# Kernel tuning notes

Hardware: AMD Instinct MI355X
Metric: run time of the kernel (lower is better)

## Reference

```python
import jax, jax.numpy as jnp
import numpy as np

SPAN = 20
REPEAT = 90


def setup_inputs() -> dict:
    key = jax.random.key(0)
    k1, k2 = jax.random.split(key)
    B, C, H, W = 4, 1, 512, 512
    pred = jax.random.normal(k1, (B, C, H, W), dtype=jnp.float32)
    gt = jax.random.normal(k2, (B, C, H, W), dtype=jnp.float32)
    # random offsets: magnitude in [1, span], random sign (matches np.random logic in torch module)
    rng = np.random.default_rng(0)
    mag_h = rng.integers(1, SPAN + 1, size=REPEAT)
    mag_w = rng.integers(1, SPAN + 1, size=REPEAT)
    sign_h = np.where(rng.uniform(size=REPEAT) > 0.5, -1, 1)
    sign_w = np.where(rng.uniform(size=REPEAT) > 0.5, -1, 1)
    h_offsets = jnp.asarray(mag_h * sign_h, dtype=jnp.int32)
    w_offsets = jnp.asarray(mag_w * sign_w, dtype=jnp.int32)
    return {"pred": pred, "gt": gt, "h_offsets": h_offsets, "w_offsets": w_offsets}


def _relative_depth(x, h_offsets, w_offsets):
    """x: [B,C,H,W] -> [B,Hb,Wb,R*C] stack of base-block minus shifted-block diffs."""
    B, C, H, W = x.shape
    Hb, Wb = H - 2 * SPAN, W - 2 * SPAN
    base = jax.lax.dynamic_slice(x, (0, 0, SPAN, SPAN), (B, C, Hb, Wb))

    def one_shift(h, w):
        shifted = jax.lax.dynamic_slice(x, (0, 0, SPAN + h, SPAN + w), (B, C, Hb, Wb))
        return base - shifted

    rd = jax.vmap(one_shift)(h_offsets, w_offsets)          # [R,B,C,Hb,Wb]
    R = rd.shape[0]
    rd = jnp.transpose(rd, (1, 0, 2, 3, 4)).reshape(B, R * C, Hb, Wb)  # concat along channel
    return jnp.transpose(rd, (0, 2, 3, 1))                   # [B,Hb,Wb,R*C]


def _l2_normalize(rd):
    norm = jnp.linalg.norm(rd, axis=-1, keepdims=True)
    norm = jnp.where(norm == 0, jnp.ones_like(norm), norm)
    return rd / norm


def reference(pred, gt, h_offsets, w_offsets):
    pred_rd = _l2_normalize(_relative_depth(pred, h_offsets, w_offsets))
    gt_rd = _l2_normalize(_relative_depth(gt, h_offsets, w_offsets))
    return jnp.mean(jnp.abs(pred_rd - gt_rd))
```

## Files before the change

### kernel.cpp

```cpp
#include <hip/hip_runtime.h>
#include <hip/hip_fp16.h>

#define SPAN 20
#define REPEAT 90


constexpr int W  = 512;
constexpr int Wb = 472;
constexpr int TJ = 64;
constexpr int TI = 8;
constexpr int TW = TJ + 2 * SPAN;
constexpr int TH = TI + 2 * SPAN;

__global__ __launch_bounds__(256) void rd_loss_kernel(
    const float* __restrict__ pred, const float* __restrict__ gt,
    const int* __restrict__ hoff, const int* __restrict__ woff,
    float* __restrict__ out)
{
    __shared__ __half2 tile[TH * TW];
    __shared__ float wsum[4];

    const int t  = threadIdx.x;
    const int bx = blockIdx.x;
    const int by = blockIdx.y;
    const int b  = blockIdx.z;
    const int I0 = by * TI;
    const int J0 = bx * TJ;

    const float* pb_ = pred + b * (W * W);
    const float* gb_ = gt   + b * (W * W);

    for (int e = t; e < TH * TW; e += 256) {
        const int row = e / TW;
        const int col = e - row * TW;
        const int gr  = I0 + row;
        int gc        = J0 + col; gc = gc < 511 ? gc : 511;
        const int gi  = gr * W + gc;
        tile[e] = __floats2half2_rn(pb_[gi], gb_[gi]);
    }
    __syncthreads();

    const int jj  = t & 63;
    const int wid = t >> 6;
    const int j   = J0 + jj;
    const bool valid = (j < Wb);

    const int base0 = (SPAN + wid) * TW + (SPAN + jj);
    const __half2 c0 = tile[base0];
    const __half2 c1 = tile[base0 + 4 * TW];

    __half2 sA0 = __floats2half2_rn(0.f, 0.f), sB0 = sA0;
    __half2 sA1 = sA0, sB1 = sA0;
    #pragma unroll 5
    for (int r = 0; r < REPEAT; r += 2) {
        const int offA = hoff[r]     * TW + woff[r];
        const int offB = hoff[r + 1] * TW + woff[r + 1];
        __half2 d;
        d = __hsub2(c0, tile[base0 + offA]);           sA0 = __hfma2(d, d, sA0);
        d = __hsub2(c1, tile[base0 + 4 * TW + offA]);  sA1 = __hfma2(d, d, sA1);
        d = __hsub2(c0, tile[base0 + offB]);           sB0 = __hfma2(d, d, sB0);
        d = __hsub2(c1, tile[base0 + 4 * TW + offB]);  sB1 = __hfma2(d, d, sB1);
    }
    const float ssp0 = __half2float(__low2half(sA0))  + __half2float(__low2half(sB0));
    const float ssg0 = __half2float(__high2half(sA0)) + __half2float(__high2half(sB0));
    const float ssp1 = __half2float(__low2half(sA1))  + __half2float(__low2half(sB1));
    const float ssg1 = __half2float(__high2half(sA1)) + __half2float(__high2half(sB1));

    const float invp0 = (ssp0 == 0.f) ? 1.f : rsqrtf(ssp0);
    const float invg0 = (ssg0 == 0.f) ? 1.f : rsqrtf(ssg0);
    const float invp1 = (ssp1 == 0.f) ? 1.f : rsqrtf(ssp1);
    const float invg1 = (ssg1 == 0.f) ? 1.f : rsqrtf(ssg1);
    const __half2 inv0 = __floats2half2_rn(invp0, invg0);
    const __half2 inv1 = __floats2half2_rn(invp1, invg1);

    float l0 = 0.f, l1 = 0.f;
    #pragma unroll 5
    for (int r = 0; r < REPEAT; r += 2) {
        const int offA = hoff[r]     * TW + woff[r];
        const int offB = hoff[r + 1] * TW + woff[r + 1];
        __half2 d, m;
        d = __hsub2(c0, tile[base0 + offA]);          m = __hmul2(d, inv0);
        l0 += fabsf(__half2float(__hsub(__low2half(m), __high2half(m))));
        d = __hsub2(c1, tile[base0 + 4 * TW + offA]); m = __hmul2(d, inv1);
        l1 += fabsf(__half2float(__hsub(__low2half(m), __high2half(m))));
        d = __hsub2(c0, tile[base0 + offB]);          m = __hmul2(d, inv0);
        l0 += fabsf(__half2float(__hsub(__low2half(m), __high2half(m))));
        d = __hsub2(c1, tile[base0 + 4 * TW + offB]); m = __hmul2(d, inv1);
        l1 += fabsf(__half2float(__hsub(__low2half(m), __high2half(m))));
    }

    float lsum = valid ? (l0 + l1) : 0.f;

    #pragma unroll
    for (int o = 32; o > 0; o >>= 1) lsum += __shfl_down(lsum, o, 64);

    const int lane = t & 63;
    if (lane == 0) wsum[wid] = lsum;
    __syncthreads();

    if (t == 0) {
        const float s = wsum[0] + wsum[1] + wsum[2] + wsum[3];
        constexpr float scale = 1.0f / (4.0f * 472.0f * 472.0f * 90.0f);
        atomicAdd(out, s * scale);
    }
}

extern "C" void kernel_launch(void* const* d_in, const int* in_sizes, int n_in,
                              void* d_out, int out_size, void* d_ws, size_t ws_size,
                              hipStream_t stream) {
    const float* pred = (const float*)d_in[0];
    const float* gt   = (const float*)d_in[1];
    const int* hoff   = (const int*)d_in[2];
    const int* woff   = (const int*)d_in[3];
    float* out = (float*)d_out;

    hipMemsetAsync(out, 0, sizeof(float), stream);

    dim3 grid(8, 59, 4);
    rd_loss_kernel<<<grid, 256, 0, stream>>>(pred, gt, hoff, woff, out);
}
```

Measured before the change: 49.72 us.

## Cache shifted diffs in registers and factor normalization out of the loss loop

```diff
diff --git a/kernel.cpp b/kernel.cpp
--- a/kernel.cpp
+++ b/kernel.cpp
@@ -40,26 +40,27 @@
     }
     __syncthreads();
 
-    const int jj  = t & 63;
-    const int wid = t >> 6;
-    const int j   = J0 + jj;
-    const bool valid = (j < Wb);
+    const int jp = t & 31;
+    const int ii = t >> 5;
+    const int jj = 2 * jp;
+    const int j0 = J0 + jj;
 
-    const int base0 = (SPAN + wid) * TW + (SPAN + jj);
+    const int base0 = (SPAN + ii) * TW + (SPAN + jj);
     const __half2 c0 = tile[base0];
-    const __half2 c1 = tile[base0 + 4 * TW];
+    const __half2 c1 = tile[base0 + 1];
 
+    __half2 d0[REPEAT], d1[REPEAT];
     __half2 sA0 = __floats2half2_rn(0.f, 0.f), sB0 = sA0;
     __half2 sA1 = sA0, sB1 = sA0;
-    #pragma unroll 5
-    for (int r = 0; r < REPEAT; r += 2) {
-        const int offA = hoff[r]     * TW + woff[r];
-        const int offB = hoff[r + 1] * TW + woff[r + 1];
-        __half2 d;
-        d = __hsub2(c0, tile[base0 + offA]);           sA0 = __hfma2(d, d, sA0);
-        d = __hsub2(c1, tile[base0 + 4 * TW + offA]);  sA1 = __hfma2(d, d, sA1);
-        d = __hsub2(c0, tile[base0 + offB]);           sB0 = __hfma2(d, d, sB0);
-        d = __hsub2(c1, tile[base0 + 4 * TW + offB]);  sB1 = __hfma2(d, d, sB1);
+    #pragma unroll
+    for (int r = 0; r < REPEAT; ++r) {
+        const int off = hoff[r] * TW + woff[r];
+        const __half2 v0 = tile[base0 + off];
+        const __half2 v1 = tile[base0 + off + 1];
+        d0[r] = __hsub2(c0, v0);
+        d1[r] = __hsub2(c1, v1);
+        if (r & 1) { sB0 = __hfma2(d0[r], d0[r], sB0); sB1 = __hfma2(d1[r], d1[r], sB1); }
+        else       { sA0 = __hfma2(d0[r], d0[r], sA0); sA1 = __hfma2(d1[r], d1[r], sA1); }
     }
     const float ssp0 = __half2float(__low2half(sA0))  + __half2float(__low2half(sB0));
     const float ssg0 = __half2float(__high2half(sA0)) + __half2float(__high2half(sB0));
@@ -70,31 +71,28 @@
     const float invg0 = (ssg0 == 0.f) ? 1.f : rsqrtf(ssg0);
     const float invp1 = (ssp1 == 0.f) ? 1.f : rsqrtf(ssp1);
     const float invg1 = (ssg1 == 0.f) ? 1.f : rsqrtf(ssg1);
-    const __half2 inv0 = __floats2half2_rn(invp0, invg0);
-    const __half2 inv1 = __floats2half2_rn(invp1, invg1);
 
-    float l0 = 0.f, l1 = 0.f;
-    #pragma unroll 5
-    for (int r = 0; r < REPEAT; r += 2) {
-        const int offA = hoff[r]     * TW + woff[r];
-        const int offB = hoff[r + 1] * TW + woff[r + 1];
-        __half2 d, m;
-        d = __hsub2(c0, tile[base0 + offA]);          m = __hmul2(d, inv0);
-        l0 += fabsf(__half2float(__hsub(__low2half(m), __high2half(m))));
-        d = __hsub2(c1, tile[base0 + 4 * TW + offA]); m = __hmul2(d, inv1);
-        l1 += fabsf(__half2float(__hsub(__low2half(m), __high2half(m))));
-        d = __hsub2(c0, tile[base0 + offB]);          m = __hmul2(d, inv0);
-        l0 += fabsf(__half2float(__hsub(__low2half(m), __high2half(m))));
-        d = __hsub2(c1, tile[base0 + 4 * TW + offB]); m = __hmul2(d, inv1);
-        l1 += fabsf(__half2float(__hsub(__low2half(m), __high2half(m))));
+    const __half nr0 = __float2half(-(invg0 / invp0));
+    const __half nr1 = __float2half(-(invg1 / invp1));
+
+    __half aA0 = __float2half(0.f), aB0 = aA0, aA1 = aA0, aB1 = aA0;
+    #pragma unroll
+    for (int r = 0; r < REPEAT; ++r) {
+        const __half s0 = __hfma(nr0, __high2half(d0[r]), __low2half(d0[r]));
+        const __half s1 = __hfma(nr1, __high2half(d1[r]), __low2half(d1[r]));
+        if (r & 1) { aB0 = __hadd(aB0, __habs(s0)); aB1 = __hadd(aB1, __habs(s1)); }
+        else       { aA0 = __hadd(aA0, __habs(s0)); aA1 = __hadd(aA1, __habs(s1)); }
     }
+    const float l0 = invp0 * (__half2float(aA0) + __half2float(aB0));
+    const float l1 = invp1 * (__half2float(aA1) + __half2float(aB1));
 
-    float lsum = valid ? (l0 + l1) : 0.f;
+    float lsum = ((j0 < Wb) ? l0 : 0.f) + ((j0 + 1 < Wb) ? l1 : 0.f);
 
     #pragma unroll
     for (int o = 32; o > 0; o >>= 1) lsum += __shfl_down(lsum, o, 64);
 
     const int lane = t & 63;
+    const int wid  = t >> 6;
     if (lane == 0) wsum[wid] = lsum;
     __syncthreads();
 
```

Result: slower. 53.48 us (+7.6%).
